# Kernel tuning notes

Hardware: AMD Instinct MI355X
Metric: run time of the kernel (lower is better)

## Reference

```python
import jax, jax.numpy as jnp
import numpy as np

D_MODEL = 512
N_HEADS = 8
D_K = 64
N_GENE = 16384
N_TF = 512


def setup_inputs() -> dict:
    key = jax.random.key(0)
    ks = jax.random.split(key, 12)
    HD = N_HEADS * D_K
    s = 1.0 / np.sqrt(D_MODEL)
    inp = {
        "H_TF": jax.random.normal(ks[0], (N_TF, D_MODEL), jnp.float32),
        "H_G": jax.random.normal(ks[1], (N_GENE, D_MODEL), jnp.float32),
        "z_exp": jax.random.normal(ks[2], (N_GENE, D_MODEL), jnp.float32),
        "z_seq": jax.random.normal(ks[3], (N_GENE, D_MODEL), jnp.float32),
        "z_txt": jax.random.normal(ks[4], (N_GENE, D_MODEL), jnp.float32),
        "tf_idx": jax.random.randint(ks[5], (N_TF,), 0, N_GENE, jnp.int64)
        if jax.config.jax_enable_x64 else jax.random.randint(ks[5], (N_TF,), 0, N_GENE, jnp.int32),
        "Wq_seq": jax.random.normal(ks[6], (D_MODEL, HD), jnp.float32) * s,
        "Wk_seq": jax.random.normal(ks[7], (D_MODEL, HD), jnp.float32) * s,
        "Wq_exp": jax.random.normal(ks[8], (D_MODEL, HD), jnp.float32) * s,
        "Wk_exp": jax.random.normal(ks[9], (D_MODEL, HD), jnp.float32) * s,
        "Wq_txt": jax.random.normal(ks[10], (D_MODEL, HD), jnp.float32) * s,
        "Wk_txt": jax.random.normal(ks[11], (D_MODEL, HD), jnp.float32) * s,
        # gate initialized as identity per head, zero bias (as in nn.init.eye_)
        "gate_weight": jnp.tile(jnp.eye(3, dtype=jnp.float32)[None], (N_HEADS, 1, 1)),
        "gate_bias": jnp.zeros((N_HEADS, 3), jnp.float32),
    }
    return inp


def reference(H_TF, H_G, z_exp, z_seq, z_txt, tf_idx,
              Wq_seq, Wk_seq, Wq_exp, Wk_exp, Wq_txt, Wk_txt,
              gate_weight, gate_bias):
    n_tf, n_gene = H_TF.shape[0], H_G.shape[0]
    H, dk = N_HEADS, D_K
    scale = jnp.sqrt(jnp.asarray(dk, H_TF.dtype))

    def qk_score(z, Wq, Wk):
        Q = (z[tf_idx] @ Wq).reshape(n_tf, H, dk)   # [t,h,d]
        K = (z @ Wk).reshape(n_gene, H, dk)          # [g,h,d]
        return jnp.einsum('thd,ghd->htg', Q, K) / scale  # [h,t,g]

    s_bind = qk_score(z_seq, Wq_seq, Wk_seq)
    s_coexpr = qk_score(z_exp, Wq_exp, Wk_exp)
    s_know = qk_score(z_txt, Wq_txt, Wk_txt)

    # evidence gate: per-head 3x3 mixing + softmax over evidence axis
    s = jnp.stack([s_bind, s_coexpr, s_know], axis=-1)        # [h,t,g,3]
    gate_logits = jnp.einsum('htge,hef->htgf', s, gate_weight) + gate_bias[:, None, None, :]
    alpha = jax.nn.softmax(gate_logits, axis=-1)               # [h,t,g,3]

    u = alpha[..., 0] * s_bind + alpha[..., 1] * s_coexpr + alpha[..., 2] * s_know
    A = jax.nn.softmax(u, axis=-1)                             # softmax over genes

    u_mean = u.mean(axis=0)          # [t,g]
    A_mean = A.mean(axis=0)          # [t,g]
    alpha_mean = alpha.mean(axis=0)  # [t,g,3]
    return (H_TF, H_G, A_mean, u_mean, alpha_mean)
```

## Files before the change

kernel.cpp:

```cpp
#include <hip/hip_runtime.h>
#include <hip/hip_bf16.h>
#include <stdint.h>

typedef __attribute__((ext_vector_type(4))) float f32x4;
typedef __attribute__((ext_vector_type(8))) short bf16x8;

#define N_GENE 16384
#define N_TF   512
#define DMODEL 512

__device__ __forceinline__ float bf2f(unsigned short u) {
    union { unsigned int i; float f; } v; v.i = ((unsigned int)u) << 16; return v.f;
}
__device__ __forceinline__ unsigned short f2bf(float f) {
    union { float f; unsigned int i; } v; v.f = f;
    unsigned int x = v.i;
    return (unsigned short)((x + 0x7fffu + ((x >> 16) & 1u)) >> 16);
}

__global__ void zerof(float* __restrict__ p, int n) {
    int i = blockIdx.x * blockDim.x + threadIdx.x;
    if (i < n) p[i] = 0.f;
}

__global__ void copy16(const int4* __restrict__ src, int4* __restrict__ dst, int n) {
    int i = blockIdx.x * blockDim.x + threadIdx.x;
    if (i < n) dst[i] = src[i];
}

__global__ void transpose6(const float* __restrict__ s0, const float* __restrict__ s1,
                           const float* __restrict__ s2, const float* __restrict__ s3,
                           const float* __restrict__ s4, const float* __restrict__ s5,
                           unsigned short* __restrict__ dst) {
    const float* srcs[6] = { s0, s1, s2, s3, s4, s5 };
    int m = blockIdx.z;
    __shared__ unsigned short tile[32][33];
    int x = blockIdx.x * 32 + threadIdx.x;
    int y0 = blockIdx.y * 32;
    const float* src = srcs[m];
    for (int i = threadIdx.y; i < 32; i += 8)
        tile[i][threadIdx.x] = f2bf(src[(size_t)(y0 + i) * 512 + x]);
    __syncthreads();
    int xo = blockIdx.y * 32 + threadIdx.x;
    int yo0 = blockIdx.x * 32;
    unsigned short* d = dst + (size_t)m * 512 * 512;
    for (int i = threadIdx.y; i < 32; i += 8)
        d[(size_t)(yo0 + i) * 512 + xo] = tile[threadIdx.x][i];
}

__global__ __launch_bounds__(256) void gemm_bt(const float* __restrict__ A,
                                               const unsigned short* __restrict__ Bt,
                                               unsigned short* __restrict__ C,
                                               const int* __restrict__ idx) {
    __shared__ unsigned short As[128 * 40];
    __shared__ unsigned short Bs[128 * 40];
    const int tid = threadIdx.x;
    const int lane = tid & 63;
    const int w = tid >> 6;
    const int mBase = blockIdx.y * 128;
    const int nBase = blockIdx.x * 128;
    const int wm = (w & 1) * 64;
    const int wn = (w >> 1) * 64;
    const int lm = lane & 15, lq = lane >> 4;

    f32x4 acc[4][4] = {};

    for (int k0 = 0; k0 < 512; k0 += 32) {
        #pragma unroll
        for (int rr = 0; rr < 2; ++rr) {
            int linear = rr * 256 + tid;
            int row = linear >> 2;
            int c8 = (linear & 3) * 8;
            int gr = mBase + row;
            int arow = idx ? idx[gr] : gr;
            float4 a0 = *(const float4*)(A + (size_t)arow * 512 + k0 + c8);
            float4 a1 = *(const float4*)(A + (size_t)arow * 512 + k0 + c8 + 4);
            unsigned short* as = As + row * 40 + c8;
            as[0] = f2bf(a0.x); as[1] = f2bf(a0.y); as[2] = f2bf(a0.z); as[3] = f2bf(a0.w);
            as[4] = f2bf(a1.x); as[5] = f2bf(a1.y); as[6] = f2bf(a1.z); as[7] = f2bf(a1.w);
            *(bf16x8*)(Bs + row * 40 + c8) = *(const bf16x8*)(Bt + (size_t)(nBase + row) * 512 + k0 + c8);
        }
        __syncthreads();
        bf16x8 af[4], bfr[4];
        #pragma unroll
        for (int mt = 0; mt < 4; ++mt)
            af[mt] = *(const bf16x8*)(As + (wm + mt * 16 + lm) * 40 + lq * 8);
        #pragma unroll
        for (int nt = 0; nt < 4; ++nt)
            bfr[nt] = *(const bf16x8*)(Bs + (wn + nt * 16 + lm) * 40 + lq * 8);
        #pragma unroll
        for (int mt = 0; mt < 4; ++mt)
            #pragma unroll
            for (int nt = 0; nt < 4; ++nt)
                acc[mt][nt] = __builtin_amdgcn_mfma_f32_16x16x32_bf16(af[mt], bfr[nt], acc[mt][nt], 0, 0, 0);
        __syncthreads();
    }
    #pragma unroll
    for (int mt = 0; mt < 4; ++mt)
        #pragma unroll
        for (int nt = 0; nt < 4; ++nt)
            #pragma unroll
            for (int r = 0; r < 4; ++r) {
                int m = mBase + wm + mt * 16 + lq * 4 + r;
                int n = nBase + wn + nt * 16 + lm;
                C[(size_t)m * 512 + n] = f2bf(acc[mt][nt][r]);
            }
}

__global__ __launch_bounds__(256) void score_pass(const unsigned short* __restrict__ Qp,
                                                  const unsigned short* __restrict__ Kp,
                                                  const float* __restrict__ gw,
                                                  const float* __restrict__ gb,
                                                  unsigned short* __restrict__ p_out,
                                                  float* __restrict__ l_out,
                                                  float* __restrict__ u_mean,
                                                  float* __restrict__ alpha_mean)
{
    const int tid = threadIdx.x;
    const int lane = tid & 63;
    const int w = tid >> 6;
    const int tw = blockIdx.y * 128 + w * 32;
    const int g0 = blockIdx.x * 32;
    const int lm = lane & 15, lq = lane >> 4;

    float u_sum[2][2][4] = {};
    float a_sum[3][2][2][4] = {};

    #pragma unroll 1
    for (int h = 0; h < 8; ++h) {
        float W[3][3], B[3];
        #pragma unroll
        for (int e = 0; e < 3; ++e)
            #pragma unroll
            for (int f = 0; f < 3; ++f) W[e][f] = gw[(h * 3 + e) * 3 + f];
        #pragma unroll
        for (int f = 0; f < 3; ++f) B[f] = gb[h * 3 + f];

        f32x4 s[3][2][2];
        #pragma unroll
        for (int e = 0; e < 3; ++e) {
            bf16x8 q[2][2], k[2][2];
            #pragma unroll
            for (int mt = 0; mt < 2; ++mt) {
                const unsigned short* qb = Qp + (size_t)e * 512 * 512 + (size_t)(tw + mt * 16 + lm) * 512 + h * 64 + lq * 8;
                q[mt][0] = *(const bf16x8*)(qb);
                q[mt][1] = *(const bf16x8*)(qb + 32);
            }
            #pragma unroll
            for (int nt = 0; nt < 2; ++nt) {
                const unsigned short* kb = Kp + (size_t)e * N_GENE * 512 + (size_t)(g0 + nt * 16 + lm) * 512 + h * 64 + lq * 8;
                k[nt][0] = *(const bf16x8*)(kb);
                k[nt][1] = *(const bf16x8*)(kb + 32);
            }
            #pragma unroll
            for (int mt = 0; mt < 2; ++mt)
                #pragma unroll
                for (int nt = 0; nt < 2; ++nt) {
                    f32x4 a = {};
                    a = __builtin_amdgcn_mfma_f32_16x16x32_bf16(q[mt][0], k[nt][0], a, 0, 0, 0);
                    a = __builtin_amdgcn_mfma_f32_16x16x32_bf16(q[mt][1], k[nt][1], a, 0, 0, 0);
                    s[e][mt][nt] = a;
                }
        }
        float lpart[2][4] = {};
        #pragma unroll
        for (int mt = 0; mt < 2; ++mt)
            #pragma unroll
            for (int nt = 0; nt < 2; ++nt)
                #pragma unroll
                for (int r = 0; r < 4; ++r) {
                    float s0 = s[0][mt][nt][r] * 0.125f;
                    float s1 = s[1][mt][nt][r] * 0.125f;
                    float s2 = s[2][mt][nt][r] * 0.125f;
                    float gl0 = s0 * W[0][0] + s1 * W[1][0] + s2 * W[2][0] + B[0];
                    float gl1 = s0 * W[0][1] + s1 * W[1][1] + s2 * W[2][1] + B[1];
                    float gl2 = s0 * W[0][2] + s1 * W[1][2] + s2 * W[2][2] + B[2];
                    float mx = fmaxf(gl0, fmaxf(gl1, gl2));
                    float e0 = __expf(gl0 - mx), e1 = __expf(gl1 - mx), e2 = __expf(gl2 - mx);
                    float rz = 1.0f / (e0 + e1 + e2);
                    float a0 = e0 * rz, a1 = e1 * rz, a2 = e2 * rz;
                    float u = a0 * s0 + a1 * s1 + a2 * s2;
                    float pv = __expf(u);
                    u_sum[mt][nt][r] += u;
                    a_sum[0][mt][nt][r] += a0; a_sum[1][mt][nt][r] += a1; a_sum[2][mt][nt][r] += a2;
                    lpart[mt][r] += pv;
                    int t = tw + mt * 16 + lq * 4 + r;
                    int g = g0 + nt * 16 + lm;
                    p_out[((size_t)h * N_TF + t) * N_GENE + g] = f2bf(pv);
                }
        #pragma unroll
        for (int mt = 0; mt < 2; ++mt)
            #pragma unroll
            for (int r = 0; r < 4; ++r) {
                float v = lpart[mt][r];
                v += __shfl_xor(v, 1);
                v += __shfl_xor(v, 2);
                v += __shfl_xor(v, 4);
                v += __shfl_xor(v, 8);
                if (lm == 0) atomicAdd(&l_out[h * N_TF + tw + mt * 16 + lq * 4 + r], v);
            }
    }
    #pragma unroll
    for (int mt = 0; mt < 2; ++mt)
        #pragma unroll
        for (int nt = 0; nt < 2; ++nt)
            #pragma unroll
            for (int r = 0; r < 4; ++r) {
                int t = tw + mt * 16 + lq * 4 + r;
                int g = g0 + nt * 16 + lm;
                u_mean[(size_t)t * N_GENE + g] = u_sum[mt][nt][r] * 0.125f;
                size_t base = ((size_t)t * N_GENE + g) * 3;
                alpha_mean[base + 0] = a_sum[0][mt][nt][r] * 0.125f;
                alpha_mean[base + 1] = a_sum[1][mt][nt][r] * 0.125f;
                alpha_mean[base + 2] = a_sum[2][mt][nt][r] * 0.125f;
            }
}

__global__ __launch_bounds__(256) void finalize_A(const unsigned short* __restrict__ p,
                                                  const float* __restrict__ l,
                                                  float* __restrict__ A_mean) {
    const int t = blockIdx.x;
    float rinv[8];
    #pragma unroll
    for (int h = 0; h < 8; ++h) rinv[h] = 0.125f / l[h * N_TF + t];
    for (int g4 = threadIdx.x * 4; g4 < N_GENE; g4 += 256 * 4) {
        float s0 = 0.f, s1 = 0.f, s2 = 0.f, s3 = 0.f;
        #pragma unroll
        for (int h = 0; h < 8; ++h) {
            ushort4 pv = *(const ushort4*)(p + ((size_t)h * N_TF + t) * N_GENE + g4);
            float r = rinv[h];
            s0 += bf2f(pv.x) * r; s1 += bf2f(pv.y) * r; s2 += bf2f(pv.z) * r; s3 += bf2f(pv.w) * r;
        }
        float4 o; o.x = s0; o.y = s1; o.z = s2; o.w = s3;
        *(float4*)(A_mean + (size_t)t * N_GENE + g4) = o;
    }
}

extern "C" void kernel_launch(void* const* d_in, const int* in_sizes, int n_in,
                              void* d_out, int out_size, void* d_ws, size_t ws_size,
                              hipStream_t stream) {
    const float* H_TF  = (const float*)d_in[0];
    const float* H_G   = (const float*)d_in[1];
    const float* z[3]  = { (const float*)d_in[3], (const float*)d_in[2], (const float*)d_in[4] };
    const int* tf_idx  = (const int*)d_in[5];
    const float* Wq[3] = { (const float*)d_in[6], (const float*)d_in[8], (const float*)d_in[10] };
    const float* Wk[3] = { (const float*)d_in[7], (const float*)d_in[9], (const float*)d_in[11] };
    const float* gw    = (const float*)d_in[12];
    const float* gb    = (const float*)d_in[13];
    float* out = (float*)d_out;

    float* out_HTF   = out;
    float* out_HG    = out + 262144;
    float* out_Amean = out + 262144 + 8388608;
    float* out_umean = out + 262144 + 8388608 + 8388608;
    float* out_alpha = out + 262144 + 8388608 + 8388608 + 8388608;

    unsigned short* Wt = (unsigned short*)d_ws;
    unsigned short* Kp = Wt + 6 * 262144;
    unsigned short* Qp = Kp + 3 * (size_t)N_GENE * 512;
    unsigned short* Pp = Qp + 3 * 512 * 512;
    float*          Lp = (float*)(Pp + (size_t)8 * N_TF * N_GENE);

    zerof<<<16, 256, 0, stream>>>(Lp, 8 * N_TF);

    transpose6<<<dim3(16, 16, 6), dim3(32, 8), 0, stream>>>(
        Wq[0], Wk[0], Wq[1], Wk[1], Wq[2], Wk[2], Wt);

    for (int e = 0; e < 3; ++e) {
        gemm_bt<<<dim3(4, 128), 256, 0, stream>>>(z[e], Wt + (size_t)(e * 2 + 1) * 262144,
                                                  Kp + (size_t)e * N_GENE * 512, nullptr);
        gemm_bt<<<dim3(4, 4), 256, 0, stream>>>(z[e], Wt + (size_t)(e * 2) * 262144,
                                                Qp + (size_t)e * 512 * 512, tf_idx);
    }

    score_pass<<<dim3(N_GENE / 32, N_TF / 128), 256, 0, stream>>>(
        Qp, Kp, gw, gb, Pp, Lp, out_umean, out_alpha);

    finalize_A<<<N_TF, 256, 0, stream>>>(Pp, Lp, out_Amean);

    copy16<<<(262144 * 4 / 16 + 255) / 256, 256, 0, stream>>>((const int4*)H_TF, (int4*)out_HTF, 262144 * 4 / 16);
    copy16<<<(8388608 * 4 / 16 + 255) / 256, 256, 0, stream>>>((const int4*)H_G, (int4*)out_HG, 8388608 * 4 / 16);
}
```

Baseline: 800.2 us.

## Pre-convert z to bf16, use direct-to-LDS GEMM loads, streamline gate math

Adds a kernel that converts the three z inputs to bf16 once, into the P workspace that is not yet in use. The projection GEMM then loads A and B tiles straight into swizzled LDS with global_load_lds, using K steps of 64. The score pass folds the scale and log2(e) into the gate weights, uses hardware exp2/rcp and drops the max-subtraction, derives the third alpha as 1-a0-a1, and sets an occupancy hint. f2bf now uses the hardware cvt instruction. Dropping the max-subtraction risks overflow for large gate logits, and the derived alpha may lose a little precision.

```diff
diff --git a/kernel.cpp b/kernel.cpp
--- a/kernel.cpp
+++ b/kernel.cpp
@@ -8,15 +8,25 @@
 #define N_GENE 16384
 #define N_TF   512
 #define DMODEL 512
+#define L2E    1.44269504088896340736f
 
 __device__ __forceinline__ float bf2f(unsigned short u) {
     union { unsigned int i; float f; } v; v.i = ((unsigned int)u) << 16; return v.f;
 }
 __device__ __forceinline__ unsigned short f2bf(float f) {
-    union { float f; unsigned int i; } v; v.f = f;
-    unsigned int x = v.i;
-    return (unsigned short)((x + 0x7fffu + ((x >> 16) & 1u)) >> 16);
-}
+    unsigned int r;
+    asm("v_cvt_pk_bf16_f32 %0, %1, %1" : "=v"(r) : "v"(f));
+    return (unsigned short)r;
+}
+__device__ __forceinline__ float fast_rcp(float x) {
+    float r; asm("v_rcp_f32 %0, %1" : "=v"(r) : "v"(x)); return r;
+}
+__device__ __forceinline__ float fast_exp2(float x) {
+    float r; asm("v_exp_f32 %0, %1" : "=v"(r) : "v"(x)); return r;
+}
+
+#define GLOBAL_AS(p) ((const __attribute__((address_space(1))) void*)(p))
+#define LDS_AS(p)    ((__attribute__((address_space(3))) void*)(p))
 
 __global__ void zerof(float* __restrict__ p, int n) {
     int i = blockIdx.x * blockDim.x + threadIdx.x;
@@ -26,6 +36,21 @@
 __global__ void copy16(const int4* __restrict__ src, int4* __restrict__ dst, int n) {
     int i = blockIdx.x * blockDim.x + threadIdx.x;
     if (i < n) dst[i] = src[i];
+}
+
+__global__ __launch_bounds__(256) void cvt3(const float* __restrict__ z0, const float* __restrict__ z1,
+                                            const float* __restrict__ z2, unsigned short* __restrict__ dst) {
+    const float* s = blockIdx.z == 0 ? z0 : (blockIdx.z == 1 ? z1 : z2);
+    size_t i = ((size_t)blockIdx.x * 256 + threadIdx.x) * 8;
+    float4 a = *(const float4*)(s + i);
+    float4 b = *(const float4*)(s + i + 4);
+    unsigned int w0, w1, w2, w3;
+    asm("v_cvt_pk_bf16_f32 %0, %1, %2" : "=v"(w0) : "v"(a.x), "v"(a.y));
+    asm("v_cvt_pk_bf16_f32 %0, %1, %2" : "=v"(w1) : "v"(a.z), "v"(a.w));
+    asm("v_cvt_pk_bf16_f32 %0, %1, %2" : "=v"(w2) : "v"(b.x), "v"(b.y));
+    asm("v_cvt_pk_bf16_f32 %0, %1, %2" : "=v"(w3) : "v"(b.z), "v"(b.w));
+    uint4 o; o.x = w0; o.y = w1; o.z = w2; o.w = w3;
+    *(uint4*)(dst + (size_t)blockIdx.z * (size_t)N_GENE * 512 + i) = o;
 }
 
 __global__ void transpose6(const float* __restrict__ s0, const float* __restrict__ s1,
@@ -48,12 +73,12 @@
         d[(size_t)(yo0 + i) * 512 + xo] = tile[threadIdx.x][i];
 }
 
-__global__ __launch_bounds__(256) void gemm_bt(const float* __restrict__ A,
-                                               const unsigned short* __restrict__ Bt,
-                                               unsigned short* __restrict__ C,
-                                               const int* __restrict__ idx) {
-    __shared__ unsigned short As[128 * 40];
-    __shared__ unsigned short Bs[128 * 40];
+__global__ __launch_bounds__(256) void gemm_bf16(const unsigned short* __restrict__ A,
+                                                 const unsigned short* __restrict__ Bt,
+                                                 unsigned short* __restrict__ C,
+                                                 const int* __restrict__ idx) {
+    __shared__ unsigned short As[128 * 64];
+    __shared__ unsigned short Bs[128 * 64];
     const int tid = threadIdx.x;
     const int lane = tid & 63;
     const int w = tid >> 6;
@@ -63,36 +88,53 @@
     const int wn = (w >> 1) * 64;
     const int lm = lane & 15, lq = lane >> 4;
 
+    const int rbase = tid >> 3;
+    const int seg = tid & 7;
+    const int scol = ((seg ^ (rbase & 7)) << 3);
+    const unsigned short* aSrc[4];
+    const unsigned short* bSrc[4];
+    #pragma unroll
+    for (int i = 0; i < 4; ++i) {
+        int r = i * 32 + rbase;
+        int ar = idx ? idx[mBase + r] : (mBase + r);
+        aSrc[i] = A + (size_t)ar * 512 + scol;
+        bSrc[i] = Bt + (size_t)(nBase + r) * 512 + scol;
+    }
+    const int ldsOfs = (tid & 192) * 8;
+
     f32x4 acc[4][4] = {};
 
-    for (int k0 = 0; k0 < 512; k0 += 32) {
-        #pragma unroll
-        for (int rr = 0; rr < 2; ++rr) {
-            int linear = rr * 256 + tid;
-            int row = linear >> 2;
-            int c8 = (linear & 3) * 8;
-            int gr = mBase + row;
-            int arow = idx ? idx[gr] : gr;
-            float4 a0 = *(const float4*)(A + (size_t)arow * 512 + k0 + c8);
-            float4 a1 = *(const float4*)(A + (size_t)arow * 512 + k0 + c8 + 4);
-            unsigned short* as = As + row * 40 + c8;
-            as[0] = f2bf(a0.x); as[1] = f2bf(a0.y); as[2] = f2bf(a0.z); as[3] = f2bf(a0.w);
-            as[4] = f2bf(a1.x); as[5] = f2bf(a1.y); as[6] = f2bf(a1.z); as[7] = f2bf(a1.w);
-            *(bf16x8*)(Bs + row * 40 + c8) = *(const bf16x8*)(Bt + (size_t)(nBase + row) * 512 + k0 + c8);
+    for (int k0 = 0; k0 < 512; k0 += 64) {
+        #pragma unroll
+        for (int i = 0; i < 4; ++i) {
+            __builtin_amdgcn_global_load_lds(GLOBAL_AS(aSrc[i] + k0), LDS_AS(As + i * 2048 + ldsOfs), 16, 0, 0);
+            __builtin_amdgcn_global_load_lds(GLOBAL_AS(bSrc[i] + k0), LDS_AS(Bs + i * 2048 + ldsOfs), 16, 0, 0);
         }
         __syncthreads();
-        bf16x8 af[4], bfr[4];
+        bf16x8 af[4][2], bfr[4][2];
+        #pragma unroll
+        for (int mt = 0; mt < 4; ++mt) {
+            int row = wm + mt * 16 + lm;
+            int sw = row & 7;
+            #pragma unroll
+            for (int hh = 0; hh < 2; ++hh)
+                af[mt][hh] = *(const bf16x8*)(As + row * 64 + (((hh * 4 + lq) ^ sw) << 3));
+        }
+        #pragma unroll
+        for (int nt = 0; nt < 4; ++nt) {
+            int row = wn + nt * 16 + lm;
+            int sw = row & 7;
+            #pragma unroll
+            for (int hh = 0; hh < 2; ++hh)
+                bfr[nt][hh] = *(const bf16x8*)(Bs + row * 64 + (((hh * 4 + lq) ^ sw) << 3));
+        }
         #pragma unroll
         for (int mt = 0; mt < 4; ++mt)
-            af[mt] = *(const bf16x8*)(As + (wm + mt * 16 + lm) * 40 + lq * 8);
-        #pragma unroll
-        for (int nt = 0; nt < 4; ++nt)
-            bfr[nt] = *(const bf16x8*)(Bs + (wn + nt * 16 + lm) * 40 + lq * 8);
-        #pragma unroll
-        for (int mt = 0; mt < 4; ++mt)
-            #pragma unroll
-            for (int nt = 0; nt < 4; ++nt)
-                acc[mt][nt] = __builtin_amdgcn_mfma_f32_16x16x32_bf16(af[mt], bfr[nt], acc[mt][nt], 0, 0, 0);
+            #pragma unroll
+            for (int nt = 0; nt < 4; ++nt) {
+                acc[mt][nt] = __builtin_amdgcn_mfma_f32_16x16x32_bf16(af[mt][0], bfr[nt][0], acc[mt][nt], 0, 0, 0);
+                acc[mt][nt] = __builtin_amdgcn_mfma_f32_16x16x32_bf16(af[mt][1], bfr[nt][1], acc[mt][nt], 0, 0, 0);
+            }
         __syncthreads();
     }
     #pragma unroll
@@ -107,14 +149,14 @@
             }
 }
 
-__global__ __launch_bounds__(256) void score_pass(const unsigned short* __restrict__ Qp,
-                                                  const unsigned short* __restrict__ Kp,
-                                                  const float* __restrict__ gw,
-                                                  const float* __restrict__ gb,
-                                                  unsigned short* __restrict__ p_out,
-                                                  float* __restrict__ l_out,
-                                                  float* __restrict__ u_mean,
-                                                  float* __restrict__ alpha_mean)
+__global__ __launch_bounds__(256, 4) void score_pass(const unsigned short* __restrict__ Qp,
+                                                     const unsigned short* __restrict__ Kp,
+                                                     const float* __restrict__ gw,
+                                                     const float* __restrict__ gb,
+                                                     unsigned short* __restrict__ p_out,
+                                                     float* __restrict__ l_out,
+                                                     float* __restrict__ u_mean,
+                                                     float* __restrict__ alpha_mean)
 {
     const int tid = threadIdx.x;
     const int lane = tid & 63;
@@ -124,33 +166,34 @@
     const int lm = lane & 15, lq = lane >> 4;
 
     float u_sum[2][2][4] = {};
-    float a_sum[3][2][2][4] = {};
+    float a0_sum[2][2][4] = {};
+    float a1_sum[2][2][4] = {};
 
     #pragma unroll 1
     for (int h = 0; h < 8; ++h) {
-        float W[3][3], B[3];
+        float W2[3][3], B2[3];
         #pragma unroll
         for (int e = 0; e < 3; ++e)
             #pragma unroll
-            for (int f = 0; f < 3; ++f) W[e][f] = gw[(h * 3 + e) * 3 + f];
-        #pragma unroll
-        for (int f = 0; f < 3; ++f) B[f] = gb[h * 3 + f];
+            for (int f = 0; f < 3; ++f) W2[e][f] = gw[(h * 3 + e) * 3 + f] * (0.125f * L2E);
+        #pragma unroll
+        for (int f = 0; f < 3; ++f) B2[f] = gb[h * 3 + f] * L2E;
 
         f32x4 s[3][2][2];
         #pragma unroll
         for (int e = 0; e < 3; ++e) {
+            const unsigned short* qbase = Qp + (size_t)e * 512 * 512 + (size_t)(tw + lm) * 512 + h * 64 + lq * 8;
+            const unsigned short* kbase = Kp + (size_t)e * N_GENE * 512 + (size_t)(g0 + lm) * 512 + h * 64 + lq * 8;
             bf16x8 q[2][2], k[2][2];
             #pragma unroll
             for (int mt = 0; mt < 2; ++mt) {
-                const unsigned short* qb = Qp + (size_t)e * 512 * 512 + (size_t)(tw + mt * 16 + lm) * 512 + h * 64 + lq * 8;
-                q[mt][0] = *(const bf16x8*)(qb);
-                q[mt][1] = *(const bf16x8*)(qb + 32);
+                q[mt][0] = *(const bf16x8*)(qbase + mt * 16 * 512);
+                q[mt][1] = *(const bf16x8*)(qbase + mt * 16 * 512 + 32);
             }
             #pragma unroll
             for (int nt = 0; nt < 2; ++nt) {
-                const unsigned short* kb = Kp + (size_t)e * N_GENE * 512 + (size_t)(g0 + nt * 16 + lm) * 512 + h * 64 + lq * 8;
-                k[nt][0] = *(const bf16x8*)(kb);
-                k[nt][1] = *(const bf16x8*)(kb + 32);
+                k[nt][0] = *(const bf16x8*)(kbase + nt * 16 * 512);
+                k[nt][1] = *(const bf16x8*)(kbase + nt * 16 * 512 + 32);
             }
             #pragma unroll
             for (int mt = 0; mt < 2; ++mt)
@@ -166,28 +209,29 @@
         #pragma unroll
         for (int mt = 0; mt < 2; ++mt)
             #pragma unroll
-            for (int nt = 0; nt < 2; ++nt)
+            for (int nt = 0; nt < 2; ++nt) {
+                unsigned short* pb = p_out + ((size_t)h * N_TF + (tw + mt * 16 + lq * 4)) * N_GENE + (g0 + nt * 16 + lm);
                 #pragma unroll
                 for (int r = 0; r < 4; ++r) {
-                    float s0 = s[0][mt][nt][r] * 0.125f;
-                    float s1 = s[1][mt][nt][r] * 0.125f;
-                    float s2 = s[2][mt][nt][r] * 0.125f;
-                    float gl0 = s0 * W[0][0] + s1 * W[1][0] + s2 * W[2][0] + B[0];
-                    float gl1 = s0 * W[0][1] + s1 * W[1][1] + s2 * W[2][1] + B[1];
-                    float gl2 = s0 * W[0][2] + s1 * W[1][2] + s2 * W[2][2] + B[2];
-                    float mx = fmaxf(gl0, fmaxf(gl1, gl2));
-                    float e0 = __expf(gl0 - mx), e1 = __expf(gl1 - mx), e2 = __expf(gl2 - mx);
-                    float rz = 1.0f / (e0 + e1 + e2);
-                    float a0 = e0 * rz, a1 = e1 * rz, a2 = e2 * rz;
-                    float u = a0 * s0 + a1 * s1 + a2 * s2;
-                    float pv = __expf(u);
+                    float s0 = s[0][mt][nt][r];
+                    float s1 = s[1][mt][nt][r];
+                    float s2 = s[2][mt][nt][r];
+                    float gl0 = fmaf(s2, W2[2][0], fmaf(s1, W2[1][0], fmaf(s0, W2[0][0], B2[0])));
+                    float gl1 = fmaf(s2, W2[2][1], fmaf(s1, W2[1][1], fmaf(s0, W2[0][1], B2[1])));
+                    float gl2 = fmaf(s2, W2[2][2], fmaf(s1, W2[1][2], fmaf(s0, W2[0][2], B2[2])));
+                    float e0 = fast_exp2(gl0), e1 = fast_exp2(gl1), e2 = fast_exp2(gl2);
+                    float rz = fast_rcp(e0 + e1 + e2);
+                    float a0 = e0 * rz, a1 = e1 * rz;
+                    float dot = fmaf(e0, s0, fmaf(e1, s1, e2 * s2));
+                    float u = dot * (rz * 0.125f);
+                    float pv = fast_exp2(u * L2E);
                     u_sum[mt][nt][r] += u;
-                    a_sum[0][mt][nt][r] += a0; a_sum[1][mt][nt][r] += a1; a_sum[2][mt][nt][r] += a2;
+                    a0_sum[mt][nt][r] += a0;
+                    a1_sum[mt][nt][r] += a1;
                     lpart[mt][r] += pv;
-                    int t = tw + mt * 16 + lq * 4 + r;
-                    int g = g0 + nt * 16 + lm;
-                    p_out[((size_t)h * N_TF + t) * N_GENE + g] = f2bf(pv);
+                    pb[(size_t)r * N_GENE] = f2bf(pv);
                 }
+            }
         #pragma unroll
         for (int mt = 0; mt < 2; ++mt)
             #pragma unroll
@@ -209,10 +253,12 @@
                 int t = tw + mt * 16 + lq * 4 + r;
                 int g = g0 + nt * 16 + lm;
                 u_mean[(size_t)t * N_GENE + g] = u_sum[mt][nt][r] * 0.125f;
+                float a0m = a0_sum[mt][nt][r] * 0.125f;
+                float a1m = a1_sum[mt][nt][r] * 0.125f;
                 size_t base = ((size_t)t * N_GENE + g) * 3;
-                alpha_mean[base + 0] = a_sum[0][mt][nt][r] * 0.125f;
-                alpha_mean[base + 1] = a_sum[1][mt][nt][r] * 0.125f;
-                alpha_mean[base + 2] = a_sum[2][mt][nt][r] * 0.125f;
+                alpha_mean[base + 0] = a0m;
+                alpha_mean[base + 1] = a1m;
+                alpha_mean[base + 2] = 1.0f - a0m - a1m;
             }
 }
 
@@ -260,17 +306,21 @@
     unsigned short* Qp = Kp + 3 * (size_t)N_GENE * 512;
     unsigned short* Pp = Qp + 3 * 512 * 512;
     float*          Lp = (float*)(Pp + (size_t)8 * N_TF * N_GENE);
+    unsigned short* Zb = Pp;
 
     zerof<<<16, 256, 0, stream>>>(Lp, 8 * N_TF);
 
     transpose6<<<dim3(16, 16, 6), dim3(32, 8), 0, stream>>>(
         Wq[0], Wk[0], Wq[1], Wk[1], Wq[2], Wk[2], Wt);
 
+    cvt3<<<dim3(N_GENE * 512 / (256 * 8), 1, 3), 256, 0, stream>>>(z[0], z[1], z[2], Zb);
+
     for (int e = 0; e < 3; ++e) {
-        gemm_bt<<<dim3(4, 128), 256, 0, stream>>>(z[e], Wt + (size_t)(e * 2 + 1) * 262144,
-                                                  Kp + (size_t)e * N_GENE * 512, nullptr);
-        gemm_bt<<<dim3(4, 4), 256, 0, stream>>>(z[e], Wt + (size_t)(e * 2) * 262144,
-                                                Qp + (size_t)e * 512 * 512, tf_idx);
+        const unsigned short* zb = Zb + (size_t)e * N_GENE * 512;
+        gemm_bf16<<<dim3(4, 128), 256, 0, stream>>>(zb, Wt + (size_t)(e * 2 + 1) * 262144,
+                                                    Kp + (size_t)e * N_GENE * 512, nullptr);
+        gemm_bf16<<<dim3(4, 4), 256, 0, stream>>>(zb, Wt + (size_t)(e * 2) * 262144,
+                                                  Qp + (size_t)e * 512 * 512, tf_idx);
     }
 
     score_pass<<<dim3(N_GENE / 32, N_TF / 128), 256, 0, stream>>>(
```

Measured after the change: 786.9 us. No clear change (-1.7%).
